# Performance work log

Hardware: AMD Instinct MI355X
Metric: run time of the kernel (lower is better)

## Reference

```python
import jax, jax.numpy as jnp
import numpy as np

POS_SCALE = 50.0
LEN_SCALE = 500.0

N_NODES = 100000
N_EDGES = 600000
IN_DIM = 128
HID_DIM = 128


def setup_inputs() -> dict:
    key = jax.random.key(0)
    ks = jax.random.split(key, 12)
    x = jax.random.normal(ks[0], (N_NODES, IN_DIM), dtype=jnp.float32)
    positions = jax.random.randint(ks[1], (N_NODES,), 0, 50, dtype=jnp.int64)
    lengths = jax.random.randint(ks[2], (N_NODES,), 0, 500, dtype=jnp.int64)
    edge_index = jax.random.randint(ks[3], (2, N_EDGES), 0, N_NODES, dtype=jnp.int64)
    reranker_scores = jax.random.normal(ks[4], (N_NODES,), dtype=jnp.float32)
    s = 1.0 / np.sqrt(IN_DIM + 2)
    fp_w = jax.random.uniform(ks[5], (IN_DIM + 2, IN_DIM), minval=-s, maxval=s, dtype=jnp.float32)
    fp_b = jnp.zeros((IN_DIM,), jnp.float32)
    s2 = 1.0 / np.sqrt(IN_DIM)
    lin_l_w = jax.random.uniform(ks[6], (IN_DIM, HID_DIM), minval=-s2, maxval=s2, dtype=jnp.float32)
    lin_l_b = jnp.zeros((HID_DIM,), jnp.float32)
    lin_r_w = jax.random.uniform(ks[7], (IN_DIM, HID_DIM), minval=-s2, maxval=s2, dtype=jnp.float32)
    res_w = jax.random.uniform(ks[8], (IN_DIM, HID_DIM), minval=-s2, maxval=s2, dtype=jnp.float32)
    res_b = jnp.zeros((HID_DIM,), jnp.float32)
    s3 = 1.0 / np.sqrt(HID_DIM)
    sh_w = jax.random.uniform(ks[9], (HID_DIM, 1), minval=-s3, maxval=s3, dtype=jnp.float32)
    sh_b = jnp.zeros((1,), jnp.float32)
    alpha = jnp.asarray(0.65, jnp.float32)
    return {
        "x": x, "positions": positions, "lengths": lengths,
        "edge_index": edge_index, "reranker_scores": reranker_scores,
        "fp_w": fp_w, "fp_b": fp_b,
        "lin_l_w": lin_l_w, "lin_l_b": lin_l_b, "lin_r_w": lin_r_w,
        "res_w": res_w, "res_b": res_b,
        "sh_w": sh_w, "sh_b": sh_b, "alpha": alpha,
    }


def reference(x, positions, lengths, edge_index, reranker_scores,
              fp_w, fp_b, lin_l_w, lin_l_b, lin_r_w, res_w, res_b,
              sh_w, sh_b, alpha):
    n = x.shape[0]
    # position/length features
    pos_feat = positions[:, None].astype(x.dtype) / POS_SCALE
    len_feat = lengths[:, None].astype(x.dtype) / LEN_SCALE
    xf = jnp.concatenate([x, pos_feat, len_feat], axis=-1)  # [N, D+2]
    xf = xf @ fp_w + fp_b                                   # [N, D]
    h_in = xf @ res_w + res_b                               # residual proj [N, H]
    # SAGEConv with mean aggregation: out = lin_l(mean_{j->i} x_j) + lin_r(x_i)
    src, dst = edge_index[0], edge_index[1]
    msg_sum = jax.ops.segment_sum(xf[src], dst, num_segments=n)          # [N, D]
    cnt = jax.ops.segment_sum(jnp.ones((src.shape[0], 1), xf.dtype), dst, num_segments=n)
    agg = msg_sum / jnp.maximum(cnt, 1.0)
    h = jax.nn.relu(agg @ lin_l_w + lin_l_b + xf @ lin_r_w)  # [N, H]
    # dropout is identity in eval mode
    h = h + h_in
    gnn_scores = (h @ sh_w + sh_b)[:, 0]                     # [N]
    a = jax.nn.sigmoid(alpha)
    return a * reranker_scores + (1.0 - a) * gnn_scores
```

## Files before the change

kernel.cpp:

```cpp
#include <hip/hip_runtime.h>
#include <hip/hip_bf16.h>
#include <cstdint>

#define D 128
#define LDSPITCH 136
#define CAP 32

typedef __attribute__((ext_vector_type(4))) float f32x4;
typedef __attribute__((ext_vector_type(2))) float f32x2;
typedef __attribute__((ext_vector_type(8))) short s16x8;

__device__ __forceinline__ unsigned short f2b(float f) {
    union { float f; uint32_t u; } v; v.f = f;
    uint32_t b = v.u + 0x7fffu + ((v.u >> 16) & 1u);
    return (unsigned short)(b >> 16);
}

#if __has_builtin(__builtin_amdgcn_cvt_pk_fp8_f32) && __has_builtin(__builtin_amdgcn_cvt_pk_f32_fp8)
__device__ __forceinline__ unsigned char f_to_fp8(float f) {
    int r = __builtin_amdgcn_cvt_pk_fp8_f32(f, 0.f, 0, false);
    return (unsigned char)(r & 0xff);
}
__device__ __forceinline__ void fp8x8_to_f32(float* o, int wx, int wy) {
    f32x2 p0 = __builtin_amdgcn_cvt_pk_f32_fp8(wx, false);
    f32x2 p1 = __builtin_amdgcn_cvt_pk_f32_fp8(wx, true);
    f32x2 p2 = __builtin_amdgcn_cvt_pk_f32_fp8(wy, false);
    f32x2 p3 = __builtin_amdgcn_cvt_pk_f32_fp8(wy, true);
    o[0] = p0.x; o[1] = p0.y; o[2] = p1.x; o[3] = p1.y;
    o[4] = p2.x; o[5] = p2.y; o[6] = p3.x; o[7] = p3.y;
}
#else
__device__ __forceinline__ unsigned char f_to_fp8(float f) {
    union { float f; uint32_t u; } v; v.f = f;
    uint32_t s = (v.u >> 31) << 7;
    uint32_t bits = v.u & 0x7fffffffu;
    if (bits < 0x3a800000u) return (unsigned char)s;
    uint32_t r = bits + 0x7ffffu + ((bits >> 20) & 1u);
    int ee = (int)(r >> 23) - 127 + 7;
    uint32_t man = (r >> 20) & 7u;
    if (ee <= 0) return (unsigned char)s;
    if (ee > 15) { ee = 15; man = 6; }
    if (ee == 15 && man == 7) man = 6;
    return (unsigned char)(s | ((uint32_t)ee << 3) | man);
}
__device__ __forceinline__ float fp8_one(unsigned char u) {
    int s = u >> 7, e = (u >> 3) & 15, m = u & 7;
    if (e == 0) { float v = (float)m * 0.001953125f; return s ? -v : v; }
    union { uint32_t u; float f; } w;
    w.u = ((uint32_t)s << 31) | ((uint32_t)(e + 120) << 23) | ((uint32_t)m << 20);
    return w.f;
}
__device__ __forceinline__ void fp8x8_to_f32(float* o, int wx, int wy) {
    uint32_t a = (uint32_t)wx, b = (uint32_t)wy;
#pragma unroll
    for (int k = 0; k < 4; ++k) o[k] = fp8_one((a >> (8 * k)) & 0xff);
#pragma unroll
    for (int k = 0; k < 4; ++k) o[4 + k] = fp8_one((b >> (8 * k)) & 0xff);
}
#endif
__device__ __forceinline__ void fp8x8_acc(float* t, int wx, int wy) {
    float o[8];
    fp8x8_to_f32(o, wx, wy);
#pragma unroll
    for (int k = 0; k < 8; ++k) t[k] += o[k];
}

__global__ __launch_bounds__(256) void k_prep(
    const float* __restrict__ fp_w, const float* __restrict__ lin_l_w,
    const float* __restrict__ lin_r_w,
    unsigned short* __restrict__ Btf, unsigned short* __restrict__ Btl,
    unsigned short* __restrict__ Btr,
    const float* __restrict__ res_w, const float* __restrict__ res_b,
    const float* __restrict__ sh_w, const float* __restrict__ sh_b,
    const float* __restrict__ alpha, float* __restrict__ c1, float* __restrict__ scal,
    int* __restrict__ cursor, int* __restrict__ srcs,
    unsigned char* __restrict__ xf8, int N, int zb) {
    int bid = blockIdx.x, tid = threadIdx.x;
    if (bid < 192) {
        int m = bid >> 6;
        int i = (bid & 63) * 256 + tid;
        const float* src = (m == 0) ? fp_w : (m == 1) ? lin_l_w : lin_r_w;
        unsigned short* dst = (m == 0) ? Btf : (m == 1) ? Btl : Btr;
        int k = i >> 7, n = i & 127;
        dst[n * D + k] = f2b(src[k * D + n]);
    } else if (bid == 192) {
        if (tid < 128) {
            float s = 0.f;
            for (int j = 0; j < D; ++j) s += res_w[tid * D + j] * sh_w[j];
            c1[tid] = s;
            if (tid == 0) {
                float c0 = 0.f;
                for (int j = 0; j < D; ++j) c0 += res_b[j] * sh_w[j];
                c0 += sh_b[0];
                float a = 1.f / (1.f + expf(-alpha[0]));
                scal[0] = a; scal[1] = c0;
            }
        } else if (tid < 160) {
            ((unsigned int*)(xf8 + (size_t)N * D))[tid - 128] = 0u;
        }
    } else if (bid < 193 + zb) {
        int i = ((bid - 193) * 256 + tid) * 4;
        if (i < N) {
            if (i + 3 < N) *(int4*)(cursor + i) = (int4){0, 0, 0, 0};
            else { for (int k = i; k < N; ++k) cursor[k] = 0; }
        }
    } else {
        int i = ((bid - 193 - zb) * 256 + tid) * 4;
        if (i < N * CAP) *(int4*)(srcs + i) = (int4){N, N, N, N};
    }
}

__global__ __launch_bounds__(256) void k_gemm1(
    const float* __restrict__ x, unsigned char* __restrict__ xf8,
    const int* __restrict__ positions, const int* __restrict__ lengths,
    const unsigned short* __restrict__ Btf,
    const float* __restrict__ fp_w, const float* __restrict__ fp_b,
    const float* __restrict__ c1, float* __restrict__ d1, int N, int mb,
    const int* __restrict__ ei, int* __restrict__ cursor, int* __restrict__ srcs, int E) {
    if (blockIdx.x >= mb) {
        int e = (blockIdx.x - mb) * 256 + threadIdx.x;
        if (e < E) {
            int src = ei[e];
            int dst = ei[E + e];
            int pos = atomicAdd(&cursor[dst], 1);
            if (pos < CAP) srcs[(size_t)pos * N + dst] = src;
        }
        return;
    }
    int lane = threadIdx.x & 63;
    int wv = threadIdx.x >> 6;
    int col = lane & 15, q = lane >> 4;
    int row0 = blockIdx.x * 64 + wv * 16;
    int arow = row0 + col; if (arow > N - 1) arow = N - 1;

    f32x4 acc[8];
#pragma unroll
    for (int nt = 0; nt < 8; ++nt) acc[nt] = (f32x4){0.f, 0.f, 0.f, 0.f};

#pragma unroll
    for (int ks = 0; ks < 4; ++ks) {
        const float* xp = x + (size_t)arow * D + ks * 32 + q * 8;
        float4 a0 = *(const float4*)xp;
        float4 a1 = *(const float4*)(xp + 4);
        s16x8 af;
        af[0] = (short)f2b(a0.x); af[1] = (short)f2b(a0.y);
        af[2] = (short)f2b(a0.z); af[3] = (short)f2b(a0.w);
        af[4] = (short)f2b(a1.x); af[5] = (short)f2b(a1.y);
        af[6] = (short)f2b(a1.z); af[7] = (short)f2b(a1.w);
#pragma unroll
        for (int nt = 0; nt < 8; ++nt) {
            s16x8 bf = *(const s16x8*)(Btf + (size_t)(nt * 16 + col) * D + ks * 32 + q * 8);
            acc[nt] = __builtin_amdgcn_mfma_f32_16x16x32_bf16(af, bf, acc[nt], 0, 0, 0);
        }
    }

    float pf[4], lf[4];
#pragma unroll
    for (int r = 0; r < 4; ++r) {
        int rr = row0 + q * 4 + r; int rc = rr < N ? rr : N - 1;
        pf[r] = (float)positions[rc] * (1.0f / 50.0f);
        lf[r] = (float)lengths[rc] * (1.0f / 500.0f);
    }
    float sdot[4] = {0.f, 0.f, 0.f, 0.f};
#pragma unroll
    for (int nt = 0; nt < 8; ++nt) {
        int n = nt * 16 + col;
        float bias = fp_b[n];
        float w128 = fp_w[128 * D + n];
        float w129 = fp_w[129 * D + n];
        float c1v = c1[n];
#pragma unroll
        for (int r = 0; r < 4; ++r) {
            float t = acc[nt][r] + bias + pf[r] * w128 + lf[r] * w129;
            int rr = row0 + q * 4 + r;
            if (rr < N) xf8[(size_t)rr * D + n] = f_to_fp8(t);
            sdot[r] += t * c1v;
        }
    }
#pragma unroll
    for (int r = 0; r < 4; ++r) {
        float s = sdot[r];
        s += __shfl_xor(s, 1, 64);
        s += __shfl_xor(s, 2, 64);
        s += __shfl_xor(s, 4, 64);
        s += __shfl_xor(s, 8, 64);
        if (col == 0) {
            int rr = row0 + q * 4 + r;
            if (rr < N) d1[rr] = s;
        }
    }
}

__global__ __launch_bounds__(256) void k_gemm2(
    const unsigned char* __restrict__ xf8,
    const int* __restrict__ cursor, const int* __restrict__ srcs,
    const unsigned short* __restrict__ Btl, const unsigned short* __restrict__ Btr,
    const float* __restrict__ lin_l_b, const float* __restrict__ sh_w,
    const float* __restrict__ rer, const float* __restrict__ d1,
    const float* __restrict__ scal, float* __restrict__ out, int N) {
    __shared__ unsigned short agg[64 * LDSPITCH];
    int lane = threadIdx.x & 63;
    int wv = threadIdx.x >> 6;
    int li = lane & 15, q = lane >> 4;
    int wrow0 = blockIdx.x * 64 + wv * 16;

    int idxA[4], idxB[4], degs[4];
    int dmax = 0;
#pragma unroll
    for (int rr = 0; rr < 4; ++rr) {
        int row = wrow0 + rr * 4 + q;
        int ok = row < N;
        int dg = ok ? cursor[ok ? row : 0] : 0;
        if (dg > CAP) dg = CAP;
        degs[rr] = dg;
        if (dg > dmax) dmax = dg;
        idxA[rr] = ok ? srcs[(size_t)li * N + row] : N;
        idxB[rr] = ok ? srcs[(size_t)(16 + li) * N + row] : N;
    }
    dmax = max(dmax, __shfl_xor(dmax, 16, 64));
    dmax = max(dmax, __shfl_xor(dmax, 32, 64));
    int rounds = (dmax + 7) >> 3;

    float t[4][8];
#pragma unroll
    for (int rr = 0; rr < 4; ++rr)
#pragma unroll
        for (int k2 = 0; k2 < 8; ++k2) t[rr][k2] = 0.f;

    int qbase = lane & 48;
    for (int jr = 0; jr < rounds; ++jr) {
        int lo = qbase + ((jr & 1) << 3);
#pragma unroll
        for (int rr = 0; rr < 4; ++rr) {
            int sel = (jr & 2) ? idxB[rr] : idxA[rr];
            int i0 = __shfl(sel, lo + 0, 64);
            int i1 = __shfl(sel, lo + 1, 64);
            int i2 = __shfl(sel, lo + 2, 64);
            int i3 = __shfl(sel, lo + 3, 64);
            int i4 = __shfl(sel, lo + 4, 64);
            int i5 = __shfl(sel, lo + 5, 64);
            int i6 = __shfl(sel, lo + 6, 64);
            int i7 = __shfl(sel, lo + 7, 64);
            int2 v0 = *(const int2*)(xf8 + (size_t)i0 * D + li * 8);
            int2 v1 = *(const int2*)(xf8 + (size_t)i1 * D + li * 8);
            int2 v2 = *(const int2*)(xf8 + (size_t)i2 * D + li * 8);
            int2 v3 = *(const int2*)(xf8 + (size_t)i3 * D + li * 8);
            int2 v4 = *(const int2*)(xf8 + (size_t)i4 * D + li * 8);
            int2 v5 = *(const int2*)(xf8 + (size_t)i5 * D + li * 8);
            int2 v6 = *(const int2*)(xf8 + (size_t)i6 * D + li * 8);
            int2 v7 = *(const int2*)(xf8 + (size_t)i7 * D + li * 8);
            fp8x8_acc(t[rr], v0.x, v0.y);
            fp8x8_acc(t[rr], v1.x, v1.y);
            fp8x8_acc(t[rr], v2.x, v2.y);
            fp8x8_acc(t[rr], v3.x, v3.y);
            fp8x8_acc(t[rr], v4.x, v4.y);
            fp8x8_acc(t[rr], v5.x, v5.y);
            fp8x8_acc(t[rr], v6.x, v6.y);
            fp8x8_acc(t[rr], v7.x, v7.y);
        }
    }

#pragma unroll
    for (int rr = 0; rr < 4; ++rr) {
        float rc = 1.0f / (float)(degs[rr] > 0 ? degs[rr] : 1);
        s16x8 o;
#pragma unroll
        for (int k2 = 0; k2 < 8; ++k2) o[k2] = (short)f2b(t[rr][k2] * rc);
        *(s16x8*)(agg + (wv * 16 + rr * 4 + q) * LDSPITCH + li * 8) = o;
    }

    int arow = wrow0 + li; if (arow > N - 1) arow = N - 1;

    f32x4 acc[8];
#pragma unroll
    for (int nt = 0; nt < 8; ++nt) acc[nt] = (f32x4){0.f, 0.f, 0.f, 0.f};

#pragma unroll
    for (int ks = 0; ks < 4; ++ks) {
        s16x8 af = *(const s16x8*)(agg + (wv * 16 + li) * LDSPITCH + ks * 32 + q * 8);
#pragma unroll
        for (int nt = 0; nt < 8; ++nt) {
            s16x8 bf = *(const s16x8*)(Btl + (size_t)(nt * 16 + li) * D + ks * 32 + q * 8);
            acc[nt] = __builtin_amdgcn_mfma_f32_16x16x32_bf16(af, bf, acc[nt], 0, 0, 0);
        }
    }
#pragma unroll
    for (int ks = 0; ks < 4; ++ks) {
        int2 raw = *(const int2*)(xf8 + (size_t)arow * D + ks * 32 + q * 8);
        float o[8];
        fp8x8_to_f32(o, raw.x, raw.y);
        s16x8 af;
#pragma unroll
        for (int k2 = 0; k2 < 8; ++k2) af[k2] = (short)f2b(o[k2]);
#pragma unroll
        for (int nt = 0; nt < 8; ++nt) {
            s16x8 bf = *(const s16x8*)(Btr + (size_t)(nt * 16 + li) * D + ks * 32 + q * 8);
            acc[nt] = __builtin_amdgcn_mfma_f32_16x16x32_bf16(af, bf, acc[nt], 0, 0, 0);
        }
    }

    float a = scal[0], c0 = scal[1];
    float sdot[4] = {0.f, 0.f, 0.f, 0.f};
#pragma unroll
    for (int nt = 0; nt < 8; ++nt) {
        int n = nt * 16 + li;
        float bias = lin_l_b[n];
        float shw = sh_w[n];
#pragma unroll
        for (int r = 0; r < 4; ++r) {
            float t2 = acc[nt][r] + bias;
            sdot[r] += fmaxf(t2, 0.f) * shw;
        }
    }
#pragma unroll
    for (int r = 0; r < 4; ++r) {
        float s = sdot[r];
        s += __shfl_xor(s, 1, 64);
        s += __shfl_xor(s, 2, 64);
        s += __shfl_xor(s, 4, 64);
        s += __shfl_xor(s, 8, 64);
        if (li == 0) {
            int rr = wrow0 + q * 4 + r;
            if (rr < N) out[rr] = a * rer[rr] + (1.f - a) * (c0 + d1[rr] + s);
        }
    }
}

extern "C" void kernel_launch(void* const* d_in, const int* in_sizes, int n_in,
                              void* d_out, int out_size, void* d_ws, size_t ws_size,
                              hipStream_t stream) {
    const float* x        = (const float*)d_in[0];
    const int*   positions= (const int*)d_in[1];
    const int*   lengths  = (const int*)d_in[2];
    const int*   ei       = (const int*)d_in[3];
    const float* rer      = (const float*)d_in[4];
    const float* fp_w     = (const float*)d_in[5];
    const float* fp_b     = (const float*)d_in[6];
    const float* lin_l_w  = (const float*)d_in[7];
    const float* lin_l_b  = (const float*)d_in[8];
    const float* lin_r_w  = (const float*)d_in[9];
    const float* res_w    = (const float*)d_in[10];
    const float* res_b    = (const float*)d_in[11];
    const float* sh_w     = (const float*)d_in[12];
    const float* sh_b     = (const float*)d_in[13];
    const float* alpha    = (const float*)d_in[14];
    int N = in_sizes[1];
    int E = in_sizes[3] / 2;
    float* out = (float*)d_out;

    char* ws = (char*)d_ws;
    size_t off = 0;
    auto alloc = [&](size_t bytes) -> void* {
        void* p = ws + off;
        off = (off + bytes + 255) & ~(size_t)255;
        return p;
    };
    unsigned char*  xf8 = (unsigned char*)alloc((size_t)(N + 1) * D);
    int* srcs    = (int*)alloc((size_t)N * CAP * 4);
    int* cursor  = (int*)alloc((size_t)N * 4);
    float* d1    = (float*)alloc((size_t)N * 4);
    unsigned short* Btf = (unsigned short*)alloc(D * D * 2);
    unsigned short* Btl = (unsigned short*)alloc(D * D * 2);
    unsigned short* Btr = (unsigned short*)alloc(D * D * 2);
    float* c1    = (float*)alloc(D * 4);
    float* scal  = (float*)alloc(16);

    int mb = (N + 63) / 64;
    int cb = (E + 255) / 256;
    int zb = (N + 1023) / 1024;
    int sb = (N * CAP / 4 + 255) / 256;

    k_prep<<<193 + zb + sb, 256, 0, stream>>>(fp_w, lin_l_w, lin_r_w, Btf, Btl, Btr,
                                              res_w, res_b, sh_w, sh_b, alpha, c1, scal,
                                              cursor, srcs, xf8, N, zb);
    k_gemm1<<<mb + cb, 256, 0, stream>>>(x, xf8, positions, lengths, Btf, fp_w, fp_b,
                                         c1, d1, N, mb, ei, cursor, srcs, E);
    k_gemm2<<<mb, 256, 0, stream>>>(xf8, cursor, srcs, Btl, Btr, lin_l_b, sh_w,
                                    rer, d1, scal, out, N);
}
```

Baseline: 260.8 us.

## Drop srcs sentinel fill and mask gathers by degree with 16-byte loads

Removes the prep pass that filled the whole N*CAP neighbor table with sentinel values. Instead, gather slots beyond each row's degree are masked to the zero row N, so uninitialized entries are never read. The gather loop is also reorganised so each lane loads 16 bytes of fp8 features for two rows (8 lanes per row) rather than 8 bytes for four rows. This saves a large memset (about 12.8 MB of writes) and widens the gather loads, at the cost of a different shuffle pattern and more accumulator registers.

New measurement: 263.8 us. Within noise of the previous version (+1.1%).

```diff
diff --git a/kernel.cpp b/kernel.cpp
--- a/kernel.cpp
+++ b/kernel.cpp
@@ -73,8 +73,7 @@
     const float* __restrict__ res_w, const float* __restrict__ res_b,
     const float* __restrict__ sh_w, const float* __restrict__ sh_b,
     const float* __restrict__ alpha, float* __restrict__ c1, float* __restrict__ scal,
-    int* __restrict__ cursor, int* __restrict__ srcs,
-    unsigned char* __restrict__ xf8, int N, int zb) {
+    int* __restrict__ cursor, unsigned char* __restrict__ xf8, int N) {
     int bid = blockIdx.x, tid = threadIdx.x;
     if (bid < 192) {
         int m = bid >> 6;
@@ -98,15 +97,12 @@
         } else if (tid < 160) {
             ((unsigned int*)(xf8 + (size_t)N * D))[tid - 128] = 0u;
         }
-    } else if (bid < 193 + zb) {
+    } else {
         int i = ((bid - 193) * 256 + tid) * 4;
         if (i < N) {
             if (i + 3 < N) *(int4*)(cursor + i) = (int4){0, 0, 0, 0};
             else { for (int k = i; k < N; ++k) cursor[k] = 0; }
         }
-    } else {
-        int i = ((bid - 193 - zb) * 256 + tid) * 4;
-        if (i < N * CAP) *(int4*)(srcs + i) = (int4){N, N, N, N};
     }
 }
 
@@ -202,71 +198,68 @@
     int lane = threadIdx.x & 63;
     int wv = threadIdx.x >> 6;
     int li = lane & 15, q = lane >> 4;
+    int o = lane >> 3, ol = lane & 7;
     int wrow0 = blockIdx.x * 64 + wv * 16;
 
-    int idxA[4], idxB[4], degs[4];
-    int dmax = 0;
-#pragma unroll
-    for (int rr = 0; rr < 4; ++rr) {
-        int row = wrow0 + rr * 4 + q;
-        int ok = row < N;
-        int dg = ok ? cursor[ok ? row : 0] : 0;
-        if (dg > CAP) dg = CAP;
-        degs[rr] = dg;
-        if (dg > dmax) dmax = dg;
-        idxA[rr] = ok ? srcs[(size_t)li * N + row] : N;
-        idxB[rr] = ok ? srcs[(size_t)(16 + li) * N + row] : N;
-    }
-    dmax = max(dmax, __shfl_xor(dmax, 16, 64));
-    dmax = max(dmax, __shfl_xor(dmax, 32, 64));
+    int rowL = wrow0 + li;
+    int okL = rowL < N;
+    int degL = okL ? cursor[okL ? rowL : 0] : 0;
+    if (degL > CAP) degL = CAP;
+    int dmax = degL;
+    dmax = max(dmax, __shfl_xor(dmax, 1, 64));
+    dmax = max(dmax, __shfl_xor(dmax, 2, 64));
+    dmax = max(dmax, __shfl_xor(dmax, 4, 64));
+    dmax = max(dmax, __shfl_xor(dmax, 8, 64));
     int rounds = (dmax + 7) >> 3;
 
-    float t[4][8];
-#pragma unroll
-    for (int rr = 0; rr < 4; ++rr)
-#pragma unroll
-        for (int k2 = 0; k2 < 8; ++k2) t[rr][k2] = 0.f;
-
-    int qbase = lane & 48;
-    for (int jr = 0; jr < rounds; ++jr) {
-        int lo = qbase + ((jr & 1) << 3);
-#pragma unroll
-        for (int rr = 0; rr < 4; ++rr) {
-            int sel = (jr & 2) ? idxB[rr] : idxA[rr];
-            int i0 = __shfl(sel, lo + 0, 64);
-            int i1 = __shfl(sel, lo + 1, 64);
-            int i2 = __shfl(sel, lo + 2, 64);
-            int i3 = __shfl(sel, lo + 3, 64);
-            int i4 = __shfl(sel, lo + 4, 64);
-            int i5 = __shfl(sel, lo + 5, 64);
-            int i6 = __shfl(sel, lo + 6, 64);
-            int i7 = __shfl(sel, lo + 7, 64);
-            int2 v0 = *(const int2*)(xf8 + (size_t)i0 * D + li * 8);
-            int2 v1 = *(const int2*)(xf8 + (size_t)i1 * D + li * 8);
-            int2 v2 = *(const int2*)(xf8 + (size_t)i2 * D + li * 8);
-            int2 v3 = *(const int2*)(xf8 + (size_t)i3 * D + li * 8);
-            int2 v4 = *(const int2*)(xf8 + (size_t)i4 * D + li * 8);
-            int2 v5 = *(const int2*)(xf8 + (size_t)i5 * D + li * 8);
-            int2 v6 = *(const int2*)(xf8 + (size_t)i6 * D + li * 8);
-            int2 v7 = *(const int2*)(xf8 + (size_t)i7 * D + li * 8);
-            fp8x8_acc(t[rr], v0.x, v0.y);
-            fp8x8_acc(t[rr], v1.x, v1.y);
-            fp8x8_acc(t[rr], v2.x, v2.y);
-            fp8x8_acc(t[rr], v3.x, v3.y);
-            fp8x8_acc(t[rr], v4.x, v4.y);
-            fp8x8_acc(t[rr], v5.x, v5.y);
-            fp8x8_acc(t[rr], v6.x, v6.y);
-            fp8x8_acc(t[rr], v7.x, v7.y);
-        }
-    }
-
-#pragma unroll
-    for (int rr = 0; rr < 4; ++rr) {
-        float rc = 1.0f / (float)(degs[rr] > 0 ? degs[rr] : 1);
-        s16x8 o;
-#pragma unroll
-        for (int k2 = 0; k2 < 8; ++k2) o[k2] = (short)f2b(t[rr][k2] * rc);
-        *(s16x8*)(agg + (wv * 16 + rr * 4 + q) * LDSPITCH + li * 8) = o;
+    int idxm[8];
+#pragma unroll
+    for (int m = 0; m < 8; ++m)
+        idxm[m] = okL ? srcs[(size_t)(m * 4 + q) * N + rowL] : N;
+
+    int degR[2];
+    degR[0] = __shfl(degL, o, 64);
+    degR[1] = __shfl(degL, 8 + o, 64);
+
+    float t0[16], t1[16];
+#pragma unroll
+    for (int k = 0; k < 16; ++k) { t0[k] = 0.f; t1[k] = 0.f; }
+
+#pragma unroll
+    for (int jr = 0; jr < 4; ++jr) {
+        if (jr >= rounds) break;
+#pragma unroll
+        for (int u = 0; u < 8; ++u) {
+            int s = jr * 8 + u;
+            const int m = 2 * jr + (u >> 2);
+            int srcl0 = ((u & 3) << 4) + o;
+            int srcl1 = ((u & 3) << 4) + 8 + o;
+            int j0 = __shfl(idxm[m], srcl0, 64);
+            int j1 = __shfl(idxm[m], srcl1, 64);
+            int i0 = (s < degR[0]) ? j0 : N;
+            int i1 = (s < degR[1]) ? j1 : N;
+            int4 v0 = *(const int4*)(xf8 + (size_t)i0 * D + ol * 16);
+            int4 v1 = *(const int4*)(xf8 + (size_t)i1 * D + ol * 16);
+            fp8x8_acc(t0, v0.x, v0.y); fp8x8_acc(t0 + 8, v0.z, v0.w);
+            fp8x8_acc(t1, v1.x, v1.y); fp8x8_acc(t1 + 8, v1.z, v1.w);
+        }
+    }
+
+    {
+        float rc0 = 1.0f / (float)(degR[0] > 0 ? degR[0] : 1);
+        float rc1 = 1.0f / (float)(degR[1] > 0 ? degR[1] : 1);
+        s16x8 a0, a1, b0, b1;
+#pragma unroll
+        for (int k = 0; k < 8; ++k) {
+            a0[k] = (short)f2b(t0[k] * rc0);
+            a1[k] = (short)f2b(t0[8 + k] * rc0);
+            b0[k] = (short)f2b(t1[k] * rc1);
+            b1[k] = (short)f2b(t1[8 + k] * rc1);
+        }
+        unsigned short* d0 = agg + (wv * 16 + o) * LDSPITCH + ol * 16;
+        unsigned short* d1p = agg + (wv * 16 + 8 + o) * LDSPITCH + ol * 16;
+        *(s16x8*)d0 = a0; *(s16x8*)(d0 + 8) = a1;
+        *(s16x8*)d1p = b0; *(s16x8*)(d1p + 8) = b1;
     }
 
     int arow = wrow0 + li; if (arow > N - 1) arow = N - 1;
@@ -287,11 +280,11 @@
 #pragma unroll
     for (int ks = 0; ks < 4; ++ks) {
         int2 raw = *(const int2*)(xf8 + (size_t)arow * D + ks * 32 + q * 8);
-        float o[8];
-        fp8x8_to_f32(o, raw.x, raw.y);
+        float ov[8];
+        fp8x8_to_f32(ov, raw.x, raw.y);
         s16x8 af;
 #pragma unroll
-        for (int k2 = 0; k2 < 8; ++k2) af[k2] = (short)f2b(o[k2]);
+        for (int k2 = 0; k2 < 8; ++k2) af[k2] = (short)f2b(ov[k2]);
 #pragma unroll
         for (int nt = 0; nt < 8; ++nt) {
             s16x8 bf = *(const s16x8*)(Btr + (size_t)(nt * 16 + li) * D + ks * 32 + q * 8);
@@ -368,11 +361,10 @@
     int mb = (N + 63) / 64;
     int cb = (E + 255) / 256;
     int zb = (N + 1023) / 1024;
-    int sb = (N * CAP / 4 + 255) / 256;
-
-    k_prep<<<193 + zb + sb, 256, 0, stream>>>(fp_w, lin_l_w, lin_r_w, Btf, Btl, Btr,
-                                              res_w, res_b, sh_w, sh_b, alpha, c1, scal,
-                                              cursor, srcs, xf8, N, zb);
+
+    k_prep<<<193 + zb, 256, 0, stream>>>(fp_w, lin_l_w, lin_r_w, Btf, Btl, Btr,
+                                         res_w, res_b, sh_w, sh_b, alpha, c1, scal,
+                                         cursor, xf8, N);
     k_gemm1<<<mb + cb, 256, 0, stream>>>(x, xf8, positions, lengths, Btf, fp_w, fp_b,
                                          c1, d1, N, mb, ei, cursor, srcs, E);
     k_gemm2<<<mb, 256, 0, stream>>>(xf8, cursor, srcs, Btl, Btr, lin_l_b, sh_w,
```
